# Kernel tuning notes

Hardware: AMD Instinct MI355X
Metric: run time of the kernel (lower is better)

The kernel has to match this reference:

```python
import jax, jax.numpy as jnp
import numpy as np

B, T, V, CI = 1024, 256, 90, 128  # batch, in_channels(=frames), joints(hardcoded 90), inter_channels
EPS = 1e-5


def _bn(x, g, b, m, v):
    # BatchNorm1d in eval mode over channel dim of (B, C, V)
    return (x - m[None, :, None]) * (g * jax.lax.rsqrt(v + EPS))[None, :, None] + b[None, :, None]


def _conv1x1(x, w, b):
    # Conv1d kernel_size=1: (B, Cin, V) x (Cout, Cin) -> (B, Cout, V)
    return jnp.einsum('btv,ct->bcv', x, w) + b[None, :, None]


def setup_inputs() -> dict:
    key = jax.random.key(0)
    ks = iter(jax.random.split(key, 64))
    def nrm(shape, scale=1.0):
        return jax.random.normal(next(ks), shape, jnp.float32) * scale
    p = {}
    p['x1'] = nrm((B, T, V))
    p['x2'] = nrm((B, T, V))
    for nm in ('g', 'th', 'ph'):
        p[nm + '_bn_g'] = 1.0 + 0.1 * nrm((T,))
        p[nm + '_bn_b'] = 0.1 * nrm((T,))
        p[nm + '_bn_m'] = 0.1 * nrm((T,))
        p[nm + '_bn_v'] = jax.random.uniform(next(ks), (T,), jnp.float32, 0.5, 1.5)
        p[nm + '_w'] = nrm((CI, T), T ** -0.5)
        p[nm + '_b'] = 0.01 * nrm((CI,))
    p['W_w'] = nrm((T, CI), CI ** -0.5)
    p['W_b'] = 0.01 * nrm((T,))
    p['W_bn_g'] = 1.0 + 0.1 * nrm((T,))
    p['W_bn_b'] = 0.1 * nrm((T,))
    p['W_bn_m'] = 0.1 * nrm((T,))
    p['W_bn_v'] = jax.random.uniform(next(ks), (T,), jnp.float32, 0.5, 1.5)
    p['qt_w'] = nrm((CI, T), T ** -0.5); p['qt_b'] = 0.01 * nrm((CI,))
    p['ks_w'] = nrm((CI, V), V ** -0.5); p['ks_b'] = 0.01 * nrm((CI,))
    p['qs_w'] = nrm((CI, V), V ** -0.5); p['qs_b'] = 0.01 * nrm((CI,))
    p['kt_w'] = nrm((CI, T), T ** -0.5); p['kt_b'] = 0.01 * nrm((CI,))
    return p


def reference(x1, x2, g_bn_g, g_bn_b, g_bn_m, g_bn_v, g_w, g_b,
              th_bn_g, th_bn_b, th_bn_m, th_bn_v, th_w, th_b,
              ph_bn_g, ph_bn_b, ph_bn_m, ph_bn_v, ph_w, ph_b,
              W_w, W_b, W_bn_g, W_bn_b, W_bn_m, W_bn_v,
              qt_w, qt_b, ks_w, ks_b, qs_w, qs_b, kt_w, kt_b):
    # non-local branch projections (note: phi is applied to x2, theta only to x1)
    g_x1 = _conv1x1(_bn(x1, g_bn_g, g_bn_b, g_bn_m, g_bn_v), g_w, g_b)       # (B,CI,V)
    g_x2 = _conv1x1(_bn(x2, g_bn_g, g_bn_b, g_bn_m, g_bn_v), g_w, g_b)
    theta_x1 = _conv1x1(_bn(x1, th_bn_g, th_bn_b, th_bn_m, th_bn_v), th_w, th_b)
    phi_x1 = _conv1x1(_bn(x2, ph_bn_g, ph_bn_b, ph_bn_m, ph_bn_v), ph_w, ph_b)

    E_t = jnp.einsum('bcv,bdv->bcd', theta_x1, phi_x1)  # (B,CI,CI) = theta_x1 @ phi_x2^T
    E_s = jnp.einsum('bcv,bcw->bvw', theta_x1, phi_x1)  # (B,V,V)  = theta_x2 @ phi_x1
    attn_time_1 = jax.nn.softmax(E_t, axis=-1)
    attn_time_2 = jax.nn.softmax(E_t.transpose(0, 2, 1), axis=-1)
    attn_space_2 = jax.nn.softmax(E_s, axis=-1)            # softmax(energy_space_1)
    attn_space_1 = jax.nn.softmax(E_s.transpose(0, 2, 1), axis=-1)

    z1 = jnp.einsum('bcd,bdv,bvw->bcw', attn_time_2, g_x1, attn_space_2)  # (B,CI,V)
    z2 = jnp.einsum('bcd,bdv,bvw->bcw', attn_time_1, g_x2, attn_space_1)

    # cross interaction (1x1 attention: softmax over singleton dim -> 1, zero grad, kept for faithfulness)
    x1m_v = x1.mean(2)   # (B,T)
    x2m_t = x2.mean(1)   # (B,V)
    x1m_t = x1.mean(1)   # (B,V)
    x2m_v = x2.mean(2)   # (B,T)
    q_time = x1m_v @ qt_w.T + qt_b
    k_space = x2m_t @ ks_w.T + ks_b
    a_t2s = jax.nn.softmax(jnp.sum(q_time * k_space, -1, keepdims=True), axis=-1)[:, 0]  # (B,) == 1
    cross_t2s = a_t2s[:, None, None] * x1m_v[:, :, None]   # (B,T,1)
    q_space = x1m_t @ qs_w.T + qs_b
    k_time = x2m_v @ kt_w.T + kt_b
    a_s2t = jax.nn.softmax(jnp.sum(q_space * k_time, -1, keepdims=True), axis=-1)[:, 0]
    cross_s2t = a_s2t[:, None, None] * x2m_t[:, None, :]   # (B,1,V)

    # W: Conv1d(CI->T,1) then BatchNorm1d(T)
    proj1 = _bn(jnp.einsum('bcv,tc->btv', z1, W_w) + W_b[None, :, None], W_bn_g, W_bn_b, W_bn_m, W_bn_v)
    proj2 = _bn(jnp.einsum('bcv,tc->btv', z2, W_w) + W_b[None, :, None], W_bn_g, W_bn_b, W_bn_m, W_bn_v)

    w1 = jax.nn.softmax(jnp.stack([x1.mean((1, 2)), cross_s2t.mean((1, 2)), proj1.mean((1, 2))], axis=1), axis=1)
    fused_x1 = (w1[:, 0, None, None] * x1 + w1[:, 1, None, None] * cross_s2t
                + w1[:, 2, None, None] * proj1)
    w2 = jax.nn.softmax(jnp.stack([x2.mean((1, 2)), cross_t2s.mean((1, 2)), proj2.mean((1, 2))], axis=1), axis=1)
    fused_x2 = (w2[:, 0, None, None] * x2 + w2[:, 1, None, None] * cross_t2s
                + w2[:, 2, None, None] * proj2)
    return fused_x1, fused_x2
```

## Files before the change

### kernel.cpp

```cpp
#include <hip/hip_runtime.h>

typedef unsigned int u32;
typedef _Float16 f16;
typedef short s16;
typedef _Float16 f16x8 __attribute__((ext_vector_type(8)));
typedef short bf16x8 __attribute__((ext_vector_type(8)));
typedef float f32x4 __attribute__((ext_vector_type(4)));

#define MFMA16(a,b,c) __builtin_amdgcn_mfma_f32_16x16x32_f16(a,b,c,0,0,0)
#define MFMABF(a,b,c) __builtin_amdgcn_mfma_f32_16x16x32_bf16(a,b,c,0,0,0)

namespace {

constexpr int VV = 90, BTV = 256*90, NB = 1024, NT = 1024;

constexpr int XT  = 0;
constexpr int UT  = 0;
constexpr int OS1 = 0;
constexpr int US  = 17408;
constexpr int G1T = 26112;
constexpr int THT = 39168;
constexpr int OS2 = 39168;
constexpr int PHT = 52224;
constexpr int X2  = 52224;
constexpr int G2T = 65280;
constexpr int M1o = 39168;
constexpr int M2o = 51456;
constexpr int Z1o = 26112;
constexpr int Z2o = 65280;
constexpr int SBASE = 78336;
constexpr int oX1MV=0, oX2MT=256, oMRT=352, oISRT=480, oMCT=608, oISCT=736,
              oMRS=864, oISRS=960, oMCS=1056, oISCS=1152, oRED1=1248, oRED2=1376, oSCAL=1504;
constexpr int oMSP = 1520;
constexpr int SWORDS = 1536;
constexpr int SMEM_BYTES = SBASE*2 + SWORDS*4;

constexpr size_t wThP=0, wGP=65536, wPhP=131072, wWP=196608,
  wBeTh=262144, wBeG=262656, wBePh=263168, wBwe=263680, wCsw=264704, wBwsum=265216;

__device__ __forceinline__ int swz(int row, int col){
  return col ^ (((row >> 3) & 3) << 4);
}

__device__ __forceinline__ f16x8 frag_ld(const f16* p, int stride){
  int l = threadIdx.x & 63;
  return *(const f16x8*)(p + (l & 15) * stride + (l >> 4) * 8);
}
__device__ __forceinline__ bf16x8 bfrag_ld(const s16* p, int stride){
  int l = threadIdx.x & 63;
  return *(const bf16x8*)(p + (l & 15) * stride + (l >> 4) * 8);
}
__device__ __forceinline__ f16x8 frag_ld_sw(const f16* p, int stride, int rowbase, int colbase){
  int l = threadIdx.x & 63;
  int row = rowbase + (l & 15);
  int col = (colbase + (l >> 4) * 8) ^ (((row >> 3) & 3) << 4);
  return *(const f16x8*)(p + row * stride + col);
}
__device__ __forceinline__ bf16x8 bfrag_ld_sw(const s16* p, int stride, int rowbase, int colbase){
  int l = threadIdx.x & 63;
  int row = rowbase + (l & 15);
  int col = (colbase + (l >> 4) * 8) ^ (((row >> 3) & 3) << 4);
  return *(const bf16x8*)(p + row * stride + col);
}
__device__ __forceinline__ s16 f2bf(float x){
  u32 u = __float_as_uint(x);
  u += 0x7FFFu + ((u >> 16) & 1u);
  return (s16)(u >> 16);
}
__device__ __forceinline__ float bf2f(s16 h){
  return __uint_as_float(((u32)(unsigned short)h) << 16);
}

__global__ void prep_weights(
    const float* __restrict__ th_w, const float* __restrict__ th_b,
    const float* __restrict__ th_bng, const float* __restrict__ th_bnb,
    const float* __restrict__ th_bnm, const float* __restrict__ th_bnv,
    const float* __restrict__ g_w, const float* __restrict__ g_b,
    const float* __restrict__ g_bng, const float* __restrict__ g_bnb,
    const float* __restrict__ g_bnm, const float* __restrict__ g_bnv,
    const float* __restrict__ ph_w, const float* __restrict__ ph_b,
    const float* __restrict__ ph_bng, const float* __restrict__ ph_bnb,
    const float* __restrict__ ph_bnm, const float* __restrict__ ph_bnv,
    const float* __restrict__ W_w, const float* __restrict__ W_b,
    const float* __restrict__ W_bng, const float* __restrict__ W_bnb,
    const float* __restrict__ W_bnm, const float* __restrict__ W_bnv,
    char* __restrict__ ws)
{
  __shared__ float red[256];
  const int b = blockIdx.x, tid = threadIdx.x;
  f16* ThP = (f16*)(ws + wThP); f16* GP = (f16*)(ws + wGP);
  f16* PhP = (f16*)(ws + wPhP); s16* WP = (s16*)(ws + wWP);
  float* beTh = (float*)(ws + wBeTh); float* beG = (float*)(ws + wBeG);
  float* bePh = (float*)(ws + wBePh); float* bwe = (float*)(ws + wBwe);
  if (b < 128){
    const int c = b, t = tid;
    {
      float s = th_bng[t] * rsqrtf(th_bnv[t] + 1e-5f);
      float d = th_bnb[t] - th_bnm[t] * s;
      float w = th_w[c*256 + t];
      ThP[c*256 + t] = (f16)(w * s);
      red[tid] = w * d; __syncthreads();
      for (int o = 128; o > 0; o >>= 1){ if (tid < o) red[tid] += red[tid+o]; __syncthreads(); }
      if (tid == 0) beTh[c] = th_b[c] + red[0];
      __syncthreads();
    }
    {
      float s = g_bng[t] * rsqrtf(g_bnv[t] + 1e-5f);
      float d = g_bnb[t] - g_bnm[t] * s;
      float w = g_w[c*256 + t];
      GP[c*256 + t] = (f16)(w * s);
      red[tid] = w * d; __syncthreads();
      for (int o = 128; o > 0; o >>= 1){ if (tid < o) red[tid] += red[tid+o]; __syncthreads(); }
      if (tid == 0) beG[c] = g_b[c] + red[0];
      __syncthreads();
    }
    {
      float s = ph_bng[t] * rsqrtf(ph_bnv[t] + 1e-5f);
      float d = ph_bnb[t] - ph_bnm[t] * s;
      float w = ph_w[c*256 + t];
      PhP[c*256 + t] = (f16)(w * s);
      red[tid] = w * d; __syncthreads();
      for (int o = 128; o > 0; o >>= 1){ if (tid < o) red[tid] += red[tid+o]; __syncthreads(); }
      if (tid == 0) bePh[c] = ph_b[c] + red[0];
    }
  } else {
    const int t = (b - 128) * 2 + (tid >> 7);
    const int c = tid & 127;
    float s = W_bng[t] * rsqrtf(W_bnv[t] + 1e-5f);
    WP[t*128 + c] = f2bf(W_w[t*128 + c] * s);
    if (c == 0) bwe[t] = (W_b[t] - W_bnm[t]) * s + W_bnb[t];
  }
}

__global__ void prep_scalars(
    const float* __restrict__ W_w,
    const float* __restrict__ W_bng, const float* __restrict__ W_bnv,
    char* __restrict__ ws)
{
  const int tid = threadIdx.x;
  float* csw = (float*)(ws + wCsw); float* bwsum = (float*)(ws + wBwsum);
  const float* bwe = (const float*)(ws + wBwe);
  if (tid < 128){
    float a = 0.f;
    for (int t = 0; t < 256; ++t){
      float s = W_bng[t] * rsqrtf(W_bnv[t] + 1e-5f);
      a += W_w[t*128 + tid] * s;
    }
    csw[tid] = a;
  } else if (tid == 128){
    float a = 0.f;
    for (int t = 0; t < 256; ++t) a += bwe[t];
    bwsum[0] = a;
  }
}

__global__ __launch_bounds__(NT, 1)
void stacif_main(const float* __restrict__ x1g, const float* __restrict__ x2g,
                 const char* __restrict__ ws, float* __restrict__ outg)
{
  extern __shared__ f16 sm[];
  float* Sf = (float*)(sm + SBASE);
  const int tid = threadIdx.x, bid = blockIdx.x;
  const int wid = tid >> 6, l = tid & 63;
  const float* __restrict__ x1b = x1g + (size_t)bid * BTV;
  const float* __restrict__ x2b = x2g + (size_t)bid * BTV;
  const f16* ThP = (const f16*)(ws + wThP);
  const f16* GP  = (const f16*)(ws + wGP);
  const f16* PhP = (const f16*)(ws + wPhP);
  const s16* WP  = (const s16*)(ws + wWP);
  const float* beTh = (const float*)(ws + wBeTh);
  const float* beG  = (const float*)(ws + wBeG);
  const float* bePh = (const float*)(ws + wBePh);
  const float* bwe  = (const float*)(ws + wBwe);
  const float* csw  = (const float*)(ws + wCsw);
  const float* bwsum = (const float*)(ws + wBwsum);
  s16* Up  = (s16*)(sm + UT);
  s16* USp = (s16*)(sm + US);

  const int tS = tid >> 2, qS = tid & 3, vB = qS * 23;

  {
    float r1[23];
    const float* p1 = x1b + tS * 90;
    #pragma unroll
    for (int j = 0; j < 23; ++j){
      int off = vB + j; off = (off < 90) ? off : 89;
      r1[j] = p1[off];
    }
    float a = 0.f;
    #pragma unroll
    for (int j = 0; j < 23; ++j) if (vB + j < 90) a += r1[j];
    a += __shfl_xor(a, 1); a += __shfl_xor(a, 2);
    if (qS == 0) Sf[oX1MV + tS] = a * (1.f/90.f);
    #pragma unroll
    for (int j = 0; j < 23; ++j){
      int v = vB + j;
      if (v < 90) sm[XT + v*272 + tS] = (f16)r1[j];
    }
  }
  {
    float r2[23];
    const float* p2 = x2b + tS * 90;
    #pragma unroll
    for (int j = 0; j < 23; ++j){
      int off = vB + j; off = (off < 90) ? off : 89;
      r2[j] = p2[off];
    }
    #pragma unroll
    for (int j = 0; j < 23; ++j){
      int v = vB + j;
      if (v < 90) sm[X2 + v*272 + tS] = (f16)r2[j];
    }
  }
  __syncthreads();

  {
    const int mat = wid >> 3;
    const int c0 = (wid & 7) * 16;
    const f16* Wm = mat ? GP : ThP;
    const float* beg = mat ? beG : beTh;
    f32x4 acc[6] = {};
    #pragma unroll
    for (int kk = 0; kk < 8; ++kk){
      f16x8 bfr = frag_ld(Wm + c0*256 + kk*32, 256);
      #pragma unroll
      for (int vt = 0; vt < 6; ++vt){
        f16x8 a = frag_ld(sm + XT + vt*16*272 + kk*32, 272);
        acc[vt] = MFMA16(a, bfr, acc[vt]);
      }
    }
    int c = c0 + (l & 15);
    float bias = beg[c];
    #pragma unroll
    for (int vt = 0; vt < 6; ++vt){
      #pragma unroll
      for (int r = 0; r < 4; ++r){
        int v = vt*16 + (l >> 4)*4 + r;
        float val = acc[vt][r] + bias;
        if (mat) ((s16*)(sm + G1T))[v*136 + c] = (v < VV) ? f2bf(val) : (s16)0;
        else     sm[THT + v*136 + swz(v, c)] = (v < VV) ? (f16)val : (f16)0.0f;
      }
    }
  }
  __syncthreads();

  if (tid < 768){
    int v = tid >> 3, p = tid & 7;
    float a = 0.f;
    for (int j = 0; j < 32; ++j) a += (float)sm[X2 + v*272 + p*32 + j];
    a += __shfl_xor(a, 1); a += __shfl_xor(a, 2); a += __shfl_xor(a, 4);
    if (p == 0 && v < VV) Sf[oX2MT + v] = a * (1.f/256.f);
  }
  {
    const int mat = wid >> 3;
    const int c0 = (wid & 7) * 16;
    const f16* Wm = mat ? GP : PhP;
    const float* beg = mat ? beG : bePh;
    f32x4 acc[6] = {};
    #pragma unroll
    for (int kk = 0; kk < 8; ++kk){
      f16x8 bfr = frag_ld(Wm + c0*256 + kk*32, 256);
      #pragma unroll
      for (int vt = 0; vt < 6; ++vt){
        f16x8 a = frag_ld(sm + X2 + vt*16*272 + kk*32, 272);
        acc[vt] = MFMA16(a, bfr, acc[vt]);
      }
    }
    __syncthreads();
    int c = c0 + (l & 15);
    float bias = beg[c];
    #pragma unroll
    for (int vt = 0; vt < 6; ++vt){
      #pragma unroll
      for (int r = 0; r < 4; ++r){
        int v = vt*16 + (l >> 4)*4 + r;
        float val = acc[vt][r] + bias;
        if (mat) ((s16*)(sm + G2T))[v*136 + c] = (v < VV) ? f2bf(val) : (s16)0;
        else     sm[PHT + v*136 + swz(v, c)] = (v < VV) ? (f16)val : (f16)0.0f;
      }
    }
  }
  __syncthreads();

  if (wid < 8){
    int c0 = wid * 16;
    int ca = c0 + (l & 15);
    f32x4 acc[8] = {};
    for (int kk = 0; kk < 3; ++kk){
      int vb = kk*32 + (l >> 4) * 8;
      int cas = swz(vb, ca);
      f16x8 a;
      #pragma unroll
      for (int bb = 0; bb < 8; ++bb) a[bb] = sm[THT + (vb + bb)*136 + cas];
      #pragma unroll
      for (int dt = 0; dt < 8; ++dt){
        int das = swz(vb, dt*16 + (l & 15));
        f16x8 bf;
        #pragma unroll
        for (int bb = 0; bb < 8; ++bb) bf[bb] = sm[PHT + (vb + bb)*136 + das];
        acc[dt] = MFMA16(a, bf, acc[dt]);
      }
    }
    #pragma unroll
    for (int dt = 0; dt < 8; ++dt){
      float m4 = fmaxf(fmaxf(acc[dt][0], acc[dt][1]), fmaxf(acc[dt][2], acc[dt][3]));
      m4 = fmaxf(m4, __shfl_xor(m4, 16));
      m4 = fmaxf(m4, __shfl_xor(m4, 32));
      if (l < 16) Up[(dt*16 + l)*136 + 128 + wid] = f2bf(m4);
    }
    #pragma unroll
    for (int r = 0; r < 4; ++r){
      float m = -3e38f;
      #pragma unroll
      for (int dt = 0; dt < 8; ++dt) m = fmaxf(m, acc[dt][r]);
      for (int sh = 1; sh < 16; sh <<= 1) m = fmaxf(m, __shfl_xor(m, sh));
      float s = 0.f;
      #pragma unroll
      for (int dt = 0; dt < 8; ++dt){ float e = __expf(acc[dt][r] - m); acc[dt][r] = e; s += e; }
      for (int sh = 1; sh < 16; sh <<= 1) s += __shfl_xor(s, sh);
      int row = c0 + (l >> 4)*4 + r;
      if ((l & 15) == 0){ Sf[oMRT + row] = m; Sf[oISRT + row] = 1.f / s; }
      #pragma unroll
      for (int dt = 0; dt < 8; ++dt) Up[row*136 + swz(row, dt*16 + (l & 15))] = f2bf(acc[dt][r]);
    }
  } else if (wid < 14){
    int v0 = (wid - 8) * 16;
    f32x4 acc[6] = {};
    for (int kk = 0; kk < 4; ++kk){
      f16x8 a = frag_ld_sw(sm + THT, 136, v0, kk*32);
      #pragma unroll
      for (int wt = 0; wt < 6; ++wt){
        f16x8 bfr = frag_ld_sw(sm + PHT, 136, wt*16, kk*32);
        acc[wt] = MFMA16(a, bfr, acc[wt]);
      }
    }
    float wmax = -3e38f;
    #pragma unroll
    for (int r = 0; r < 4; ++r){
      float m = 0.f;
      #pragma unroll
      for (int wt = 0; wt < 6; ++wt) m = fmaxf(m, acc[wt][r]);
      for (int sh = 1; sh < 16; sh <<= 1) m = fmaxf(m, __shfl_xor(m, sh));
      float s = 0.f;
      #pragma unroll
      for (int wt = 0; wt < 6; ++wt){
        float e = __expf(acc[wt][r] - m);
        bool valid = (wt*16 + (l & 15)) < VV;
        acc[wt][r] = valid ? e : 0.f;
        s += acc[wt][r];
      }
      for (int sh = 1; sh < 16; sh <<= 1) s += __shfl_xor(s, sh);
      int row = v0 + (l >> 4)*4 + r;
      if ((l & 15) == 0){ Sf[oMRS + row] = m; Sf[oISRS + row] = 1.f / s; }
      if (row < VV) wmax = fmaxf(wmax, m);
      if (row < VV){
        #pragma unroll
        for (int wt = 0; wt < 6; ++wt) USp[row*96 + wt*16 + (l & 15)] = f2bf(acc[wt][r]);
      }
    }
    wmax = fmaxf(wmax, __shfl_xor(wmax, 16));
    wmax = fmaxf(wmax, __shfl_xor(wmax, 32));
    if (l == 0) Sf[oMSP + (wid - 8)] = wmax;
  }
  __syncthreads();

  {
    int ch = wid >> 1;
    int c = (wid & 1) * 64 + l;
    bf16x8 pm8 = *(const bf16x8*)(Up + c*136 + 128);
    float mp = bf2f(pm8[0]);
    #pragma unroll
    for (int q = 1; q < 8; ++q) mp = fmaxf(mp, bf2f(pm8[q]));
    float s = 0.f;
    #pragma unroll
    for (int j = 0; j < 16; ++j){
      int d = ch*16 + j;
      float u = bf2f(Up[d*136 + swz(d, c)]);
      if (u > 0.f){
        float e1 = __expf(0.5f * (Sf[oMRT + d] - mp));
        s += (u * e1) * e1;
      }
    }
    float* PT = (float*)(sm + THT);
    PT[ch*128 + c] = s;
    if (ch == 0) PT[1024 + c] = mp;
  }
  if (tid < 768){
    int v = tid >> 3, p = tid & 7;
    float Ms = Sf[oMSP + 0];
    #pragma unroll
    for (int q = 1; q < 6; ++q) Ms = fmaxf(Ms, Sf[oMSP + q]);
    float s = 0.f;
    for (int j = 0; j < 12; ++j){
      int w = p*12 + j;
      if (w < VV){
        float u = bf2f(USp[w*96 + v]);
        if (u > 0.f) s += u * __expf(Sf[oMRS + w] - Ms);
      }
    }
    s += __shfl_xor(s, 1); s += __shfl_xor(s, 2); s += __shfl_xor(s, 4);
    if (p == 0) Sf[oISCS + v] = 1.f / fmaxf(s, 1e-30f);
  }
  if (tid == 0){
    float Ms = Sf[oMSP + 0];
    #pragma unroll
    for (int q = 1; q < 6; ++q) Ms = fmaxf(Ms, Sf[oMSP + q]);
    Sf[oSCAL + 8] = Ms;
  }
  __syncthreads();
  if (tid < 128){
    const float* PT = (const float*)(sm + THT);
    float s = 0.f;
    #pragma unroll
    for (int q = 0; q < 8; ++q) s += PT[q*128 + tid];
    Sf[oMCT + tid] = PT[1024 + tid];
    Sf[oISCT + tid] = 1.f / s;
  }
  __syncthreads();

  if (wid < 8){
    int c0 = wid * 16;
    const s16* G1 = (const s16*)(sm + G1T);
    s16* M1 = (s16*)(sm + M1o);
    int ca = c0 + (l & 15);
    float mctc = Sf[oMCT + ca];
    f32x4 acc[6] = {};
    #pragma unroll
    for (int kk = 0; kk < 4; ++kk){
      int db = kk*32 + (l >> 4) * 8;
      int cas = swz(db, ca);
      bf16x8 a;
      #pragma unroll
      for (int bb = 0; bb < 8; ++bb){
        float u = bf2f(Up[(db + bb)*136 + cas]);
        float val = 0.f;
        if (u > 0.f){
          float e1 = __expf(0.5f * (Sf[oMRT + db + bb] - mctc));
          val = (u * e1) * e1;
        }
        a[bb] = f2bf(val);
      }
      #pragma unroll
      for (int vt = 0; vt < 6; ++vt){
        bf16x8 bfv = bfrag_ld(G1 + vt*16*136 + kk*32, 136);
        acc[vt] = MFMABF(a, bfv, acc[vt]);
      }
    }
    #pragma unroll
    for (int vt = 0; vt < 6; ++vt){
      int v = vt*16 + (l & 15);
      float cs = (v < VV) ? Sf[oISRS + v] : 0.f;
      #pragma unroll
      for (int r = 0; r < 4; ++r){
        int c = c0 + (l >> 4)*4 + r;
        M1[c*96 + v] = f2bf(acc[vt][r] * Sf[oISCT + c] * cs);
      }
    }
  } else {
    int c0 = (wid - 8) * 16;
    const s16* G2 = (const s16*)(sm + G2T);
    s16* M2 = (s16*)(sm + M2o);
    f32x4 acc[6] = {};
    #pragma unroll
    for (int kk = 0; kk < 4; ++kk){
      bf16x8 a = bfrag_ld_sw(Up, 136, c0, kk*32);
      #pragma unroll
      for (int vt = 0; vt < 6; ++vt){
        bf16x8 bfv = bfrag_ld(G2 + vt*16*136 + kk*32, 136);
        acc[vt] = MFMABF(a, bfv, acc[vt]);
      }
    }
    #pragma unroll
    for (int vt = 0; vt < 6; ++vt){
      int v = vt*16 + (l & 15);
      float cs = (v < VV) ? Sf[oISCS + v] : 0.f;
      #pragma unroll
      for (int r = 0; r < 4; ++r){
        int c = c0 + (l >> 4)*4 + r;
        M2[c*96 + v] = f2bf(acc[vt][r] * Sf[oISRT + c] * cs);
      }
    }
  }
  __syncthreads();

  for (int pass = 0; pass < 3; ++pass){
    int u = wid + pass*16;
    bool isZ2 = u >= 24;
    int rem = isZ2 ? u - 24 : u;
    int w0 = (rem >> 2) * 16;
    int cq = rem & 3;
    int wa = w0 + (l & 15);
    const s16* Mx = (const s16*)(sm + (isZ2 ? M2o : M1o));
    s16* Z = (s16*)(sm + (isZ2 ? Z2o : Z1o));
    int wr = (wa < VV) ? wa : (VV - 1);
    float e_row = isZ2 ? __expf(Sf[oMRS + wr] - Sf[oSCAL + 8]) : 0.f;
    f32x4 acc[2] = {};
    #pragma unroll
    for (int kk = 0; kk < 3; ++kk){
      int vb = kk*32 + (l >> 4) * 8;
      bf16x8 a;
      if (!isZ2){
        #pragma unroll
        for (int bb = 0; bb < 8; ++bb){
          int v = vb + bb;
          a[bb] = (v < VV) ? USp[v*96 + wa] : (s16)0;
        }
      } else {
        const s16* up = USp + wr*96 + vb;
        #pragma unroll
        for (int bb = 0; bb < 8; ++bb){
          a[bb] = f2bf(bf2f(up[bb]) * e_row);
        }
      }
      #pragma unroll
      for (int ct = 0; ct < 2; ++ct){
        bf16x8 bfv = bfrag_ld(Mx + (cq*2 + ct)*16*96 + kk*32, 96);
        acc[ct] = MFMABF(a, bfv, acc[ct]);
      }
    }
    #pragma unroll
    for (int ct = 0; ct < 2; ++ct){
      #pragma unroll
      for (int r = 0; r < 4; ++r){
        int row = w0 + (l >> 4)*4 + r;
        Z[row*136 + (cq*2 + ct)*16 + (l & 15)] = f2bf(acc[ct][r]);
      }
    }
  }
  __syncthreads();

  {
    int col = tid >> 3, zi = (tid >> 2) & 1, p = tid & 3;
    const s16* Z = (const s16*)(sm + (zi ? Z2o : Z1o));
    float s = 0.f;
    for (int j = 0; j < 23; ++j){
      int w = p*23 + j;
      if (w < VV) s += bf2f(Z[w*136 + col]);
    }
    s += __shfl_xor(s, 1); s += __shfl_xor(s, 2);
    if (p == 0){
      float* R = Sf + (zi ? oRED2 : oRED1);
      R[col] = csw[col] * s;
    }
  }
  __syncthreads();
  if (wid == 0){
    float s1 = Sf[oRED1 + l] + Sf[oRED1 + 64 + l];
    float s2 = Sf[oRED2 + l] + Sf[oRED2 + 64 + l];
    float t1 = Sf[oX1MV + l] + Sf[oX1MV + 64 + l] + Sf[oX1MV + 128 + l] + Sf[oX1MV + 192 + l];
    float t2 = (l < VV) ? Sf[oX2MT + l] : 0.f;
    if (l < 26) t2 += Sf[oX2MT + 64 + l];
    for (int sh = 1; sh < 64; sh <<= 1){
      s1 += __shfl_xor(s1, sh);
      s2 += __shfl_xor(s2, sh);
      t1 += __shfl_xor(t1, sh);
      t2 += __shfl_xor(t2, sh);
    }
    if (l == 0){
      float m1 = t1 * (1.f/256.f);
      float m2 = t2 * (1.f/90.f);
      float bws = bwsum[0];
      float mp1 = (s1 + 90.f*bws) * (1.f/23040.f);
      float mp2 = (s2 + 90.f*bws) * (1.f/23040.f);
      {
        float mx = fmaxf(m1, fmaxf(m2, mp1));
        float e0 = __expf(m1-mx), e1 = __expf(m2-mx), e2 = __expf(mp1-mx);
        float inv = 1.f/(e0+e1+e2);
        Sf[oSCAL+0] = e0*inv; Sf[oSCAL+1] = e1*inv; Sf[oSCAL+2] = e2*inv;
      }
      {
        float mx = fmaxf(m2, fmaxf(m1, mp2));
        float e0 = __expf(m2-mx), e1 = __expf(m1-mx), e2 = __expf(mp2-mx);
        float inv = 1.f/(e0+e1+e2);
        Sf[oSCAL+3] = e0*inv; Sf[oSCAL+4] = e1*inv; Sf[oSCAL+5] = e2*inv;
      }
    }
  }
  __syncthreads();

  for (int pass = 0; pass < 2; ++pass){
    int u = wid + pass*16;
    bool is2 = u & 1;
    int t0 = (u >> 1) * 16;
    const s16* Zp = (const s16*)(sm + (is2 ? Z2o : Z1o));
    f32x4 acc[6] = {};
    #pragma unroll
    for (int kk = 0; kk < 4; ++kk){
      bf16x8 a = bfrag_ld(WP + t0*128 + kk*32, 128);
      #pragma unroll
      for (int vt = 0; vt < 6; ++vt){
        bf16x8 bfr = bfrag_ld(Zp + vt*16*136 + kk*32, 136);
        acc[vt] = MFMABF(a, bfr, acc[vt]);
      }
    }
    f16* OS = sm + (is2 ? OS2 : OS1);
    float wb = is2 ? Sf[oSCAL+4] : Sf[oSCAL+1];
    float wc = is2 ? Sf[oSCAL+5] : Sf[oSCAL+2];
    #pragma unroll
    for (int r = 0; r < 4; ++r){
      int t = t0 + (l >> 4)*4 + r;
      float bw = bwe[t];
      float crossv = is2 ? Sf[oX1MV + t] : 0.f;
      #pragma unroll
      for (int vt = 0; vt < 6; ++vt){
        int v = vt*16 + (l & 15);
        if (v < VV){
          float cross = is2 ? crossv : Sf[oX2MT + v];
          OS[t*90 + v] = (f16)(wb * cross + wc * (acc[vt][r] + bw));
        }
      }
    }
  }
  __syncthreads();

  {
    float* out1 = outg + (size_t)bid * BTV;
    float* out2 = outg + (size_t)NB * BTV + (size_t)bid * BTV;
    const float4* x14 = (const float4*)x1b;
    const float4* x24 = (const float4*)x2b;
    float wa1 = Sf[oSCAL+0], wa2 = Sf[oSCAL+3];
    #pragma unroll
    for (int k = 0; k < 3; ++k){
      int e = (k*1024 + tid) * 8;
      if (e < BTV){
        float4 xa = x14[e/4], xb4 = x14[e/4 + 1];
        float4 xc = x24[e/4], xd4 = x24[e/4 + 1];
        f16x8 h1 = *(const f16x8*)(sm + OS1 + e);
        f16x8 h2 = *(const f16x8*)(sm + OS2 + e);
        float4 a1 = {wa1*xa.x + (float)h1[0], wa1*xa.y + (float)h1[1],
                     wa1*xa.z + (float)h1[2], wa1*xa.w + (float)h1[3]};
        float4 b1 = {wa1*xb4.x + (float)h1[4], wa1*xb4.y + (float)h1[5],
                     wa1*xb4.z + (float)h1[6], wa1*xb4.w + (float)h1[7]};
        float4 a2 = {wa2*xc.x + (float)h2[0], wa2*xc.y + (float)h2[1],
                     wa2*xc.z + (float)h2[2], wa2*xc.w + (float)h2[3]};
        float4 b2 = {wa2*xd4.x + (float)h2[4], wa2*xd4.y + (float)h2[5],
                     wa2*xd4.z + (float)h2[6], wa2*xd4.w + (float)h2[7]};
        *(float4*)(out1 + e)     = a1;
        *(float4*)(out1 + e + 4) = b1;
        *(float4*)(out2 + e)     = a2;
        *(float4*)(out2 + e + 4) = b2;
      }
    }
  }
}

}

extern "C" void kernel_launch(void* const* d_in, const int* in_sizes, int n_in,
                              void* d_out, int out_size, void* d_ws, size_t ws_size,
                              hipStream_t stream)
{
  (void)in_sizes; (void)n_in; (void)out_size; (void)ws_size;
  hipFuncSetAttribute((const void*)stacif_main,
                      hipFuncAttributeMaxDynamicSharedMemorySize, SMEM_BYTES);

  const float* x1 = (const float*)d_in[0];
  const float* x2 = (const float*)d_in[1];
  const float* g_bng = (const float*)d_in[2];
  const float* g_bnb = (const float*)d_in[3];
  const float* g_bnm = (const float*)d_in[4];
  const float* g_bnv = (const float*)d_in[5];
  const float* g_w   = (const float*)d_in[6];
  const float* g_b   = (const float*)d_in[7];
  const float* th_bng = (const float*)d_in[8];
  const float* th_bnb = (const float*)d_in[9];
  const float* th_bnm = (const float*)d_in[10];
  const float* th_bnv = (const float*)d_in[11];
  const float* th_w   = (const float*)d_in[12];
  const float* th_b   = (const float*)d_in[13];
  const float* ph_bng = (const float*)d_in[14];
  const float* ph_bnb = (const float*)d_in[15];
  const float* ph_bnm = (const float*)d_in[16];
  const float* ph_bnv = (const float*)d_in[17];
  const float* ph_w   = (const float*)d_in[18];
  const float* ph_b   = (const float*)d_in[19];
  const float* W_w    = (const float*)d_in[20];
  const float* W_b    = (const float*)d_in[21];
  const float* W_bng  = (const float*)d_in[22];
  const float* W_bnb  = (const float*)d_in[23];
  const float* W_bnm  = (const float*)d_in[24];
  const float* W_bnv  = (const float*)d_in[25];
  char* ws = (char*)d_ws;
  float* out = (float*)d_out;

  prep_weights<<<dim3(256), dim3(256), 0, stream>>>(
      th_w, th_b, th_bng, th_bnb, th_bnm, th_bnv,
      g_w, g_b, g_bng, g_bnb, g_bnm, g_bnv,
      ph_w, ph_b, ph_bng, ph_bnb, ph_bnm, ph_bnv,
      W_w, W_b, W_bng, W_bnb, W_bnm, W_bnv, ws);
  prep_scalars<<<dim3(1), dim3(256), 0, stream>>>(W_w, W_bng, W_bnv, ws);
  stacif_main<<<dim3(NB), dim3(NT), SMEM_BYTES, stream>>>(x1, x2, ws, out);
}
```

Before: 257.6 us.

## Pad LDS row stride to 104 and fold scalar prep into weight prep kernel

Changes the shared-memory row stride of the US, M1 and M2 bf16 tiles from 96 to 104 elements to reduce LDS bank conflicts on MFMA fragment loads. It relocates the shared buffers and reuses scratch slots to fit the padding. The single-block prep_scalars kernel is folded into prep_weights as per-block reductions, saving a launch and a serial loop. The Z2 row load also becomes one vector load. The cost is a slightly larger LDS footprint plus extra barriers inside the prep kernel.

After: 240.7 us. 1.07x faster.

```diff
diff --git a/kernel.cpp b/kernel.cpp
--- a/kernel.cpp
+++ b/kernel.cpp
@@ -18,21 +18,21 @@
 constexpr int UT  = 0;
 constexpr int OS1 = 0;
 constexpr int US  = 17408;
-constexpr int G1T = 26112;
-constexpr int THT = 39168;
-constexpr int OS2 = 39168;
-constexpr int PHT = 52224;
-constexpr int X2  = 52224;
-constexpr int G2T = 65280;
-constexpr int M1o = 39168;
-constexpr int M2o = 51456;
-constexpr int Z1o = 26112;
-constexpr int Z2o = 65280;
-constexpr int SBASE = 78336;
+constexpr int G1T = 26768;
+constexpr int THT = 39824;
+constexpr int PHT = 52880;
+constexpr int X2  = 52880;
+constexpr int G2T = 66448;
+constexpr int M1o = 39824;
+constexpr int M2o = 53136;
+constexpr int Z1o = 26768;
+constexpr int Z2o = 66448;
+constexpr int OS2 = 39824;
+constexpr int SBASE = 79504;
 constexpr int oX1MV=0, oX2MT=256, oMRT=352, oISRT=480, oMCT=608, oISCT=736,
-              oMRS=864, oISRS=960, oMCS=1056, oISCS=1152, oRED1=1248, oRED2=1376, oSCAL=1504;
-constexpr int oMSP = 1520;
-constexpr int SWORDS = 1536;
+              oMRS=864, oISRS=960, oISCS=1056, oSCAL=1152, oMSP=1168;
+constexpr int oRED1=608, oRED2=736;
+constexpr int SWORDS = 1184;
 constexpr int SMEM_BYTES = SBASE*2 + SWORDS*4;
 
 constexpr size_t wThP=0, wGP=65536, wPhP=131072, wWP=196608,
@@ -92,6 +92,7 @@
   f16* PhP = (f16*)(ws + wPhP); s16* WP = (s16*)(ws + wWP);
   float* beTh = (float*)(ws + wBeTh); float* beG = (float*)(ws + wBeG);
   float* bePh = (float*)(ws + wBePh); float* bwe = (float*)(ws + wBwe);
+  float* csw = (float*)(ws + wCsw); float* bwsum = (float*)(ws + wBwsum);
   if (b < 128){
     const int c = b, t = tid;
     {
@@ -126,31 +127,24 @@
   } else {
     const int t = (b - 128) * 2 + (tid >> 7);
     const int c = tid & 127;
-    float s = W_bng[t] * rsqrtf(W_bnv[t] + 1e-5f);
-    WP[t*128 + c] = f2bf(W_w[t*128 + c] * s);
-    if (c == 0) bwe[t] = (W_b[t] - W_bnm[t]) * s + W_bnb[t];
-  }
-}
-
-__global__ void prep_scalars(
-    const float* __restrict__ W_w,
-    const float* __restrict__ W_bng, const float* __restrict__ W_bnv,
-    char* __restrict__ ws)
-{
-  const int tid = threadIdx.x;
-  float* csw = (float*)(ws + wCsw); float* bwsum = (float*)(ws + wBwsum);
-  const float* bwe = (const float*)(ws + wBwe);
-  if (tid < 128){
-    float a = 0.f;
-    for (int t = 0; t < 256; ++t){
-      float s = W_bng[t] * rsqrtf(W_bnv[t] + 1e-5f);
-      a += W_w[t*128 + tid] * s;
-    }
-    csw[tid] = a;
-  } else if (tid == 128){
-    float a = 0.f;
-    for (int t = 0; t < 256; ++t) a += bwe[t];
-    bwsum[0] = a;
+    float sW = W_bng[t] * rsqrtf(W_bnv[t] + 1e-5f);
+    WP[t*128 + c] = f2bf(W_w[t*128 + c] * sW);
+    if (c == 0) bwe[t] = (W_b[t] - W_bnm[t]) * sW + W_bnb[t];
+    {
+      const int c2 = b - 128;
+      float sT = W_bng[tid] * rsqrtf(W_bnv[tid] + 1e-5f);
+      red[tid] = W_w[tid*128 + c2] * sT;
+      __syncthreads();
+      for (int o = 128; o > 0; o >>= 1){ if (tid < o) red[tid] += red[tid+o]; __syncthreads(); }
+      if (tid == 0) csw[c2] = red[0];
+      __syncthreads();
+      if (b == 128){
+        red[tid] = (W_b[tid] - W_bnm[tid]) * sT + W_bnb[tid];
+        __syncthreads();
+        for (int o = 128; o > 0; o >>= 1){ if (tid < o) red[tid] += red[tid+o]; __syncthreads(); }
+        if (tid == 0) bwsum[0] = red[0];
+      }
+    }
   }
 }
 
@@ -355,7 +349,7 @@
       if (row < VV) wmax = fmaxf(wmax, m);
       if (row < VV){
         #pragma unroll
-        for (int wt = 0; wt < 6; ++wt) USp[row*96 + wt*16 + (l & 15)] = f2bf(acc[wt][r]);
+        for (int wt = 0; wt < 6; ++wt) USp[row*104 + wt*16 + (l & 15)] = f2bf(acc[wt][r]);
       }
     }
     wmax = fmaxf(wmax, __shfl_xor(wmax, 16));
@@ -394,7 +388,7 @@
     for (int j = 0; j < 12; ++j){
       int w = p*12 + j;
       if (w < VV){
-        float u = bf2f(USp[w*96 + v]);
+        float u = bf2f(USp[w*104 + v]);
         if (u > 0.f) s += u * __expf(Sf[oMRS + w] - Ms);
       }
     }
@@ -453,7 +447,7 @@
       #pragma unroll
       for (int r = 0; r < 4; ++r){
         int c = c0 + (l >> 4)*4 + r;
-        M1[c*96 + v] = f2bf(acc[vt][r] * Sf[oISCT + c] * cs);
+        M1[c*104 + v] = f2bf(acc[vt][r] * Sf[oISCT + c] * cs);
       }
     }
   } else {
@@ -477,7 +471,7 @@
       #pragma unroll
       for (int r = 0; r < 4; ++r){
         int c = c0 + (l >> 4)*4 + r;
-        M2[c*96 + v] = f2bf(acc[vt][r] * Sf[oISRT + c] * cs);
+        M2[c*104 + v] = f2bf(acc[vt][r] * Sf[oISRT + c] * cs);
       }
     }
   }
@@ -503,18 +497,18 @@
         #pragma unroll
         for (int bb = 0; bb < 8; ++bb){
           int v = vb + bb;
-          a[bb] = (v < VV) ? USp[v*96 + wa] : (s16)0;
+          a[bb] = (v < VV) ? USp[v*104 + wa] : (s16)0;
         }
       } else {
-        const s16* up = USp + wr*96 + vb;
+        bf16x8 uv = *(const bf16x8*)(USp + wr*104 + vb);
         #pragma unroll
         for (int bb = 0; bb < 8; ++bb){
-          a[bb] = f2bf(bf2f(up[bb]) * e_row);
+          a[bb] = f2bf(bf2f(uv[bb]) * e_row);
         }
       }
       #pragma unroll
       for (int ct = 0; ct < 2; ++ct){
-        bf16x8 bfv = bfrag_ld(Mx + (cq*2 + ct)*16*96 + kk*32, 96);
+        bf16x8 bfv = bfrag_ld(Mx + (cq*2 + ct)*16*104 + kk*32, 104);
         acc[ct] = MFMABF(a, bfv, acc[ct]);
       }
     }
@@ -688,6 +682,5 @@
       g_w, g_b, g_bng, g_bnb, g_bnm, g_bnv,
       ph_w, ph_b, ph_bng, ph_bnb, ph_bnm, ph_bnv,
       W_w, W_b, W_bng, W_bnb, W_bnm, W_bnv, ws);
-  prep_scalars<<<dim3(1), dim3(256), 0, stream>>>(W_w, W_bng, W_bnv, ws);
   stacif_main<<<dim3(NB), dim3(NT), SMEM_BYTES, stream>>>(x1, x2, ws, out);
 }
```
